# Performance work log

Hardware: AMD Instinct MI355X
Metric: run time of the kernel (lower is better)

Reference implementation:

```python
import jax, jax.numpy as jnp
import numpy as np

N = 200000       # nodes
E = 6400000      # edges
F_IN, H1, H2, C = 7, 32, 16, 2


def gcn_conv(x, W, b, src, dst, n):
    """PyG GCNConv: add self-loops, symmetric normalization, linear, scatter-add."""
    loop = jnp.arange(n, dtype=src.dtype)
    s = jnp.concatenate([src, loop])
    d = jnp.concatenate([dst, loop])
    # degree of target nodes (with self-loops)
    deg = jax.ops.segment_sum(jnp.ones_like(d, dtype=x.dtype), d, num_segments=n)
    dinv = jnp.where(deg > 0, jax.lax.rsqrt(deg), 0.0)
    h = x @ W                                  # [n, out]
    norm = dinv[s] * dinv[d]                   # [e+n]
    msg = h[s] * norm[:, None]                 # gather + normalize
    out = jax.ops.segment_sum(msg, d, num_segments=n)  # scatter-add aggregation
    return out + b


def setup_inputs() -> dict:
    key = jax.random.key(0)
    ks = jax.random.split(key, 8)
    x = jax.random.normal(ks[0], (N, F_IN), dtype=jnp.float32)
    edge_index = jax.random.randint(ks[1], (2, E), 0, N, dtype=jnp.int64)
    def glorot(k, fan_in, fan_out):
        lim = np.sqrt(6.0 / (fan_in + fan_out)).astype(np.float32)
        return jax.random.uniform(k, (fan_in, fan_out), jnp.float32, -lim, lim)
    return {
        "x": x,
        "edge_index": edge_index,
        "W1": glorot(ks[2], F_IN, H1), "b1": jnp.zeros((H1,), jnp.float32),
        "W2": glorot(ks[3], H1, H2), "b2": jnp.zeros((H2,), jnp.float32),
        "Wfc": glorot(ks[4], H2, C), "bfc": jnp.zeros((C,), jnp.float32),
    }


def reference(x, edge_index, W1, b1, W2, b2, Wfc, bfc):
    src, dst = edge_index[0], edge_index[1]
    h = jax.nn.relu(gcn_conv(x, W1, b1, src, dst, N))
    h = jax.nn.relu(gcn_conv(h, W2, b2, src, dst, N))
    return h @ Wfc + bfc
```

## Files before the change

### kernel.cpp

```cpp
#include <hip/hip_runtime.h>

#define NNODES 200000
#define NEDGES 6400000
#define FIN 7
#define FH1 32
#define FH2 16
#define NC 2

#define WB 128
#define WB_SHIFT 7
#define NBUCK ((NNODES + WB - 1) / WB)
#define NBLK 512
#define CHUNK ((NEDGES + NBLK - 1) / NBLK)
#define PSHIFT 18
#define SRCMASK ((1u << PSHIFT) - 1)

#define SCAP 5120

#define SCAN_N (NBUCK * NBLK)
#define SCAN_ITEMS 16
#define SCAN_TILE (256 * SCAN_ITEMS)
#define SCAN_NT ((SCAN_N + SCAN_TILE - 1) / SCAN_TILE)


__global__ __launch_bounds__(256) void p1_count(const int* __restrict__ ei,
                                                int* __restrict__ counts) {
    __shared__ int h[NBUCK];
    for (int i = threadIdx.x; i < NBUCK; i += 256) h[i] = 0;
    __syncthreads();
    int base = blockIdx.x * CHUNK;
    int end = base + CHUNK;
    if (end > NEDGES) end = NEDGES;
    for (int e = base + threadIdx.x; e < end; e += 256) {
        int d = ei[NEDGES + e];
        atomicAdd(&h[d >> WB_SHIFT], 1);
    }
    __syncthreads();
    for (int i = threadIdx.x; i < NBUCK; i += 256)
        counts[i * NBLK + blockIdx.x] = h[i];
}


__global__ __launch_bounds__(256) void scan_sums(const int* __restrict__ in,
                                                 int* __restrict__ part) {
    int base = blockIdx.x * SCAN_TILE + threadIdx.x * SCAN_ITEMS;
    int s = 0;
#pragma unroll
    for (int k = 0; k < SCAN_ITEMS; ++k) {
        int idx = base + k;
        if (idx < SCAN_N) s += in[idx];
    }
    __shared__ int sm[256];
    sm[threadIdx.x] = s;
    __syncthreads();
    for (int off = 128; off > 0; off >>= 1) {
        if (threadIdx.x < off) sm[threadIdx.x] += sm[threadIdx.x + off];
        __syncthreads();
    }
    if (threadIdx.x == 0) part[blockIdx.x] = sm[0];
}

__global__ void scan_top_g(int* __restrict__ part) {
    if (threadIdx.x == 0 && blockIdx.x == 0) {
        int acc = 0;
        for (int i = 0; i < SCAN_NT; ++i) {
            int v = part[i];
            part[i] = acc;
            acc += v;
        }
    }
}

__global__ __launch_bounds__(256) void scan_write_g(const int* __restrict__ in,
                                                    const int* __restrict__ part,
                                                    int* __restrict__ out) {
    int t = threadIdx.x;
    int base = blockIdx.x * SCAN_TILE + t * SCAN_ITEMS;
    int local[SCAN_ITEMS];
    int s = 0;
#pragma unroll
    for (int k = 0; k < SCAN_ITEMS; ++k) {
        int idx = base + k;
        int v = (idx < SCAN_N) ? in[idx] : 0;
        local[k] = v;
        s += v;
    }
    __shared__ int sm[256];
    sm[t] = s;
    __syncthreads();
    for (int off = 1; off < 256; off <<= 1) {
        int v = (t >= off) ? sm[t - off] : 0;
        __syncthreads();
        sm[t] += v;
        __syncthreads();
    }
    int prefix = part[blockIdx.x] + sm[t] - s;
#pragma unroll
    for (int k = 0; k < SCAN_ITEMS; ++k) {
        int idx = base + k;
        if (idx < SCAN_N) {
            out[idx] = prefix;
            prefix += local[k];
        }
    }
}


__global__ __launch_bounds__(256) void p2_scatter(const int* __restrict__ ei,
                                                  const int* __restrict__ offs,
                                                  unsigned int* __restrict__ recs) {
    __shared__ int sorted[CHUNK];
    __shared__ int lcur[NBUCK];
    __shared__ int gbase[NBUCK];
    __shared__ int sm[256];
    int t = threadIdx.x;
    int blk = blockIdx.x;

    for (int b = t; b < NBUCK; b += 256) {
        int g = offs[b * NBLK + blk];
        gbase[b] = g;
        int nxt;
        if (blk + 1 < NBLK) nxt = offs[b * NBLK + blk + 1];
        else nxt = (b + 1 < NBUCK) ? offs[(b + 1) * NBLK] : NEDGES;
        lcur[b] = nxt - g;
    }
    __syncthreads();

    int base7 = t * 7;
    int loc[7];
    int s = 0;
#pragma unroll
    for (int k = 0; k < 7; ++k) {
        int idx = base7 + k;
        int v = (idx < NBUCK) ? lcur[idx] : 0;
        loc[k] = v;
        s += v;
    }
    sm[t] = s;
    __syncthreads();
    for (int off = 1; off < 256; off <<= 1) {
        int v = (t >= off) ? sm[t - off] : 0;
        __syncthreads();
        sm[t] += v;
        __syncthreads();
    }
    int run = sm[t] - s;
#pragma unroll
    for (int k = 0; k < 7; ++k) {
        int idx = base7 + k;
        if (idx < NBUCK) { lcur[idx] = run; run += loc[k]; }
    }
    __syncthreads();

    int ebase = blk * CHUNK;
    for (int e = ebase + t; e < ebase + CHUNK; e += 256) {
        int src = ei[e];
        int d = ei[NEDGES + e];
        int b = d >> WB_SHIFT;
        int slot = atomicAdd(&lcur[b], 1);
        sorted[slot] = (int)((unsigned)src | ((unsigned)(d & (WB - 1)) << PSHIFT));
    }
    __syncthreads();

    for (int i = t; i < CHUNK; i += 256) {
        int lo = 0, hi = NBUCK - 1;
        while (lo < hi) {
            int mid = (lo + hi) >> 1;
            if (lcur[mid] > i) hi = mid; else lo = mid + 1;
        }
        int b = lo;
        int start = (b > 0) ? lcur[b - 1] : 0;
        recs[gbase[b] + (i - start)] = (unsigned)sorted[i];
    }
}


__global__ __launch_bounds__(256) void p3_dinv(const unsigned int* __restrict__ recs,
                                               const int* __restrict__ offs,
                                               float* __restrict__ dinv) {
    __shared__ int h[WB];
    int b = blockIdx.x;
    if (threadIdx.x < WB) h[threadIdx.x] = 0;
    __syncthreads();
    int beg = offs[b * NBLK];
    int end = (b + 1 < NBUCK) ? offs[(b + 1) * NBLK] : NEDGES;
    for (int e = beg + threadIdx.x; e < end; e += 256)
        atomicAdd(&h[recs[e] >> PSHIFT], 1);
    __syncthreads();
    int node = b * WB + threadIdx.x;
    if (threadIdx.x < WB && node < NNODES)
        dinv[node] = rsqrtf((float)(1 + h[threadIdx.x]));
}


__global__ __launch_bounds__(256) void gx_kernel(const float* __restrict__ x,
                                                 const float* __restrict__ dinv,
                                                 float4* __restrict__ gx) {
    int i = blockIdx.x * blockDim.x + threadIdx.x;
    if (i >= NNODES) return;
    float di = dinv[i];
    const float* xr = x + (size_t)i * FIN;
    float4 v0, v1;
    v0.x = xr[0] * di; v0.y = xr[1] * di; v0.z = xr[2] * di; v0.w = xr[3] * di;
    v1.x = xr[4] * di; v1.y = xr[5] * di; v1.z = xr[6] * di; v1.w = 0.0f;
    gx[(size_t)i * 2 + 0] = v0;
    gx[(size_t)i * 2 + 1] = v1;
}


__global__ __launch_bounds__(256) void l1_sorted(const unsigned int* __restrict__ recs,
                                                 const int* __restrict__ offs,
                                                 const float4* __restrict__ gx,
                                                 const float* __restrict__ dinv,
                                                 const float* __restrict__ W1,
                                                 const float* __restrict__ b1,
                                                 const float* __restrict__ W2,
                                                 float4* __restrict__ y) {
    __shared__ int sl_src[SCAP];
    __shared__ int hist[WB], st[WB], cur[WB];
    __shared__ float acc[WB][9];
    __shared__ float sW1[FIN * FH1];
    __shared__ float sb1[FH1];
    __shared__ float sW2[FH1 * FH2];
    int t = threadIdx.x;
    for (int i = t; i < FIN * FH1; i += 256) sW1[i] = W1[i];
    if (t < FH1) sb1[t] = b1[t];
    for (int i = t; i < FH1 * FH2; i += 256) sW2[i] = W2[i];
    if (t < WB) hist[t] = 0;
    __syncthreads();

    int b = blockIdx.x;
    int beg = offs[b * NBLK];
    int end = (b + 1 < NBUCK) ? offs[(b + 1) * NBLK] : NEDGES;

    for (int e = beg + t; e < end; e += 256)
        atomicAdd(&hist[recs[e] >> PSHIFT], 1);
    __syncthreads();

    if (t < WB) cur[t] = hist[t];
    __syncthreads();
    for (int off = 1; off < WB; off <<= 1) {
        int v = 0;
        if (t < WB && t >= off) v = cur[t - off];
        __syncthreads();
        if (t < WB) cur[t] += v;
        __syncthreads();
    }
    if (t < WB) {
        st[t] = cur[t] - hist[t];
        cur[t] = cur[t] - hist[t];
    }
    __syncthreads();

    for (int e = beg + t; e < end; e += 256) {
        unsigned r = recs[e];
        int slot = atomicAdd(&cur[r >> PSHIFT], 1);
        sl_src[slot] = (int)(r & SRCMASK);
    }
    __syncthreads();

    int n = t >> 1;
    int hq = t & 1;
    int cnt = hist[n];
    int base = st[n];
    float ax = 0.0f, ay = 0.0f, az = 0.0f, aw = 0.0f;
    int k = 0;
    for (; k + 3 < cnt; k += 4) {
        int s0 = sl_src[base + k];
        int s1 = sl_src[base + k + 1];
        int s2 = sl_src[base + k + 2];
        int s3 = sl_src[base + k + 3];
        float4 v0 = gx[(size_t)s0 * 2 + hq];
        float4 v1 = gx[(size_t)s1 * 2 + hq];
        float4 v2 = gx[(size_t)s2 * 2 + hq];
        float4 v3 = gx[(size_t)s3 * 2 + hq];
        ax += v0.x + v1.x; ay += v0.y + v1.y;
        az += v0.z + v1.z; aw += v0.w + v1.w;
        ax += v2.x + v3.x; ay += v2.y + v3.y;
        az += v2.z + v3.z; aw += v2.w + v3.w;
    }
    for (; k < cnt; ++k) {
        int s0 = sl_src[base + k];
        float4 v0 = gx[(size_t)s0 * 2 + hq];
        ax += v0.x; ay += v0.y; az += v0.z; aw += v0.w;
    }
    int kb = hq * 4;
    acc[n][kb + 0] = ax; acc[n][kb + 1] = ay;
    acc[n][kb + 2] = az; acc[n][kb + 3] = aw;
    __syncthreads();

    int node = b * WB + t;
    if (t >= WB || node >= NNODES) return;

    float di = dinv[node];
    float4 g0 = gx[(size_t)node * 2], g1 = gx[(size_t)node * 2 + 1];
    float xa[FIN];
    xa[0] = (acc[t][0] + g0.x) * di;
    xa[1] = (acc[t][1] + g0.y) * di;
    xa[2] = (acc[t][2] + g0.z) * di;
    xa[3] = (acc[t][3] + g0.w) * di;
    xa[4] = (acc[t][4] + g1.x) * di;
    xa[5] = (acc[t][5] + g1.y) * di;
    xa[6] = (acc[t][6] + g1.z) * di;

    float h1[FH1];
#pragma unroll
    for (int j = 0; j < FH1; ++j) h1[j] = sb1[j];
#pragma unroll
    for (int f = 0; f < FIN; ++f) {
        float xv = xa[f];
#pragma unroll
        for (int j = 0; j < FH1; ++j) h1[j] = fmaf(xv, sW1[f * FH1 + j], h1[j]);
    }
#pragma unroll
    for (int j = 0; j < FH1; ++j) h1[j] = fmaxf(h1[j], 0.0f);

    float yv[FH2];
#pragma unroll
    for (int j = 0; j < FH2; ++j) yv[j] = 0.0f;
#pragma unroll
    for (int k2 = 0; k2 < FH1; ++k2) {
        float hv = h1[k2];
#pragma unroll
        for (int j = 0; j < FH2; ++j) yv[j] = fmaf(hv, sW2[k2 * FH2 + j], yv[j]);
    }

    size_t yb = (size_t)node * 4;
    float4 o;
    o.x = yv[0] * di; o.y = yv[1] * di; o.z = yv[2] * di; o.w = yv[3] * di;
    y[yb + 0] = o;
    o.x = yv[4] * di; o.y = yv[5] * di; o.z = yv[6] * di; o.w = yv[7] * di;
    y[yb + 1] = o;
    o.x = yv[8] * di; o.y = yv[9] * di; o.z = yv[10] * di; o.w = yv[11] * di;
    y[yb + 2] = o;
    o.x = yv[12] * di; o.y = yv[13] * di; o.z = yv[14] * di; o.w = yv[15] * di;
    y[yb + 3] = o;
}


__global__ __launch_bounds__(256) void l2_sorted(const unsigned int* __restrict__ recs,
                                                 const int* __restrict__ offs,
                                                 const float4* __restrict__ y,
                                                 const float* __restrict__ dinv,
                                                 const float* __restrict__ b2,
                                                 const float* __restrict__ Wfc,
                                                 const float* __restrict__ bfc,
                                                 float2* __restrict__ out) {
    __shared__ int sl_src[SCAP];
    __shared__ int hist[WB], st[WB], cur[WB];
    __shared__ float acc[WB][17];
    __shared__ float sb2[FH2];
    __shared__ float sWfc[FH2 * NC];
    __shared__ float sbfc[NC];
    int t = threadIdx.x;
    if (t < FH2) sb2[t] = b2[t];
    if (t < FH2 * NC) sWfc[t] = Wfc[t];
    if (t < NC) sbfc[t] = bfc[t];
    if (t < WB) hist[t] = 0;
    __syncthreads();

    int b = blockIdx.x;
    int beg = offs[b * NBLK];
    int end = (b + 1 < NBUCK) ? offs[(b + 1) * NBLK] : NEDGES;

    for (int e = beg + t; e < end; e += 256)
        atomicAdd(&hist[recs[e] >> PSHIFT], 1);
    __syncthreads();

    if (t < WB) cur[t] = hist[t];
    __syncthreads();
    for (int off = 1; off < WB; off <<= 1) {
        int v = 0;
        if (t < WB && t >= off) v = cur[t - off];
        __syncthreads();
        if (t < WB) cur[t] += v;
        __syncthreads();
    }
    if (t < WB) {
        st[t] = cur[t] - hist[t];
        cur[t] = cur[t] - hist[t];
    }
    __syncthreads();

    for (int e = beg + t; e < end; e += 256) {
        unsigned r = recs[e];
        int slot = atomicAdd(&cur[r >> PSHIFT], 1);
        sl_src[slot] = (int)(r & SRCMASK);
    }
    __syncthreads();

    int q = t & 3;
#pragma unroll
    for (int r = 0; r < 2; ++r) {
        int n = (t >> 2) + 64 * r;
        int cnt = hist[n];
        int base = st[n];
        float ax = 0.0f, ay = 0.0f, az = 0.0f, aw = 0.0f;
        int k = 0;
        for (; k + 3 < cnt; k += 4) {
            int s0 = sl_src[base + k];
            int s1 = sl_src[base + k + 1];
            int s2 = sl_src[base + k + 2];
            int s3 = sl_src[base + k + 3];
            float4 v0 = y[(size_t)s0 * 4 + q];
            float4 v1 = y[(size_t)s1 * 4 + q];
            float4 v2 = y[(size_t)s2 * 4 + q];
            float4 v3 = y[(size_t)s3 * 4 + q];
            ax += v0.x + v1.x; ay += v0.y + v1.y;
            az += v0.z + v1.z; aw += v0.w + v1.w;
            ax += v2.x + v3.x; ay += v2.y + v3.y;
            az += v2.z + v3.z; aw += v2.w + v3.w;
        }
        for (; k < cnt; ++k) {
            int s0 = sl_src[base + k];
            float4 v0 = y[(size_t)s0 * 4 + q];
            ax += v0.x; ay += v0.y; az += v0.z; aw += v0.w;
        }
        int kb = q * 4;
        acc[n][kb + 0] = ax; acc[n][kb + 1] = ay;
        acc[n][kb + 2] = az; acc[n][kb + 3] = aw;
    }
    __syncthreads();

    int node = b * WB + t;
    if (t >= WB || node >= NNODES) return;

    float di = dinv[node];
    size_t yb = (size_t)node * 4;
    float4 s0 = y[yb + 0], s1 = y[yb + 1], s2 = y[yb + 2], s3 = y[yb + 3];
    float self[FH2] = {s0.x, s0.y, s0.z, s0.w, s1.x, s1.y, s1.z, s1.w,
                       s2.x, s2.y, s2.z, s2.w, s3.x, s3.y, s3.z, s3.w};

    float o0 = sbfc[0], o1 = sbfc[1];
#pragma unroll
    for (int k = 0; k < FH2; ++k) {
        float h = fmaxf(fmaf(di, acc[t][k] + self[k], sb2[k]), 0.0f);
        o0 = fmaf(h, sWfc[k * NC + 0], o0);
        o1 = fmaf(h, sWfc[k * NC + 1], o1);
    }
    float2 ov; ov.x = o0; ov.y = o1;
    out[node] = ov;
}


extern "C" void kernel_launch(void* const* d_in, const int* in_sizes, int n_in,
                              void* d_out, int out_size, void* d_ws, size_t ws_size,
                              hipStream_t stream) {
    const float* x   = (const float*)d_in[0];
    const int*   ei  = (const int*)d_in[1];
    const float* W1  = (const float*)d_in[2];
    const float* b1  = (const float*)d_in[3];
    const float* W2  = (const float*)d_in[4];
    const float* b2  = (const float*)d_in[5];
    const float* Wfc = (const float*)d_in[6];
    const float* bfc = (const float*)d_in[7];
    float* out = (float*)d_out;

    char* p = (char*)d_ws;
    auto carve = [&](size_t bytes) -> char* {
        char* r = p;
        p += (bytes + 255) & ~(size_t)255;
        return r;
    };
    int*      counts = (int*)carve((size_t)SCAN_N * 4);
    int*      part   = (int*)carve(256 * 4);
    float*    dinv   = (float*)carve((size_t)NNODES * 4);
    float*    gx     = (float*)carve((size_t)NNODES * 8 * 4);
    float*    y      = (float*)carve((size_t)NNODES * 16 * 4);
    unsigned* recs   = (unsigned*)carve((size_t)NEDGES * 4);
    int* offs = counts;

    int nblocks = (NNODES + 255) / 256;

    p1_count<<<NBLK, 256, 0, stream>>>(ei, counts);
    scan_sums<<<SCAN_NT, 256, 0, stream>>>(counts, part);
    scan_top_g<<<1, 64, 0, stream>>>(part);
    scan_write_g<<<SCAN_NT, 256, 0, stream>>>(counts, part, offs);
    p2_scatter<<<NBLK, 256, 0, stream>>>(ei, offs, recs);
    p3_dinv<<<NBUCK, 256, 0, stream>>>(recs, offs, dinv);
    gx_kernel<<<nblocks, 256, 0, stream>>>(x, dinv, (float4*)gx);
    l1_sorted<<<NBUCK, 256, 0, stream>>>(recs, offs, (const float4*)gx, dinv,
                                         W1, b1, W2, (float4*)y);
    l2_sorted<<<NBUCK, 256, 0, stream>>>(recs, offs, (const float4*)y, dinv,
                                         b2, Wfc, bfc, (float2*)out);
}
```

Baseline: 382.1 us.

## Sort edges per node once in a fused pass and reuse CSR offsets in both layers

A new pass, p2b_sort, does the within-bucket counting sort once. It writes the fully node-sorted source indices back into recs, builds a per-node CSR offset array, and computes the dinv-scaled input features, replacing the separate dinv and gx kernels. The two layer kernels then skip their own histogram, scan and shared-memory scatter. They just copy the contiguous slice into shared memory and recompute dinv from the offsets. This removes duplicated edge passes and shared atomics in l1 and l2, at the cost of one extra write of recs.

```diff
diff --git a/kernel.cpp b/kernel.cpp
--- a/kernel.cpp
+++ b/kernel.cpp
@@ -175,49 +175,75 @@
 }
 
 
-__global__ __launch_bounds__(256) void p3_dinv(const unsigned int* __restrict__ recs,
-                                               const int* __restrict__ offs,
-                                               float* __restrict__ dinv) {
-    __shared__ int h[WB];
+__global__ __launch_bounds__(256) void p2b_sort(unsigned int* __restrict__ recs,
+                                                const int* __restrict__ offs,
+                                                const float* __restrict__ x,
+                                                int* __restrict__ node_off,
+                                                float4* __restrict__ gx) {
+    __shared__ int sorted[SCAP];
+    __shared__ int hist[WB], st[WB], cur[WB];
+    int t = threadIdx.x;
     int b = blockIdx.x;
-    if (threadIdx.x < WB) h[threadIdx.x] = 0;
-    __syncthreads();
+    if (t < WB) hist[t] = 0;
+    __syncthreads();
+
     int beg = offs[b * NBLK];
     int end = (b + 1 < NBUCK) ? offs[(b + 1) * NBLK] : NEDGES;
-    for (int e = beg + threadIdx.x; e < end; e += 256)
-        atomicAdd(&h[recs[e] >> PSHIFT], 1);
-    __syncthreads();
-    int node = b * WB + threadIdx.x;
-    if (threadIdx.x < WB && node < NNODES)
-        dinv[node] = rsqrtf((float)(1 + h[threadIdx.x]));
-}
-
-
-__global__ __launch_bounds__(256) void gx_kernel(const float* __restrict__ x,
-                                                 const float* __restrict__ dinv,
-                                                 float4* __restrict__ gx) {
-    int i = blockIdx.x * blockDim.x + threadIdx.x;
-    if (i >= NNODES) return;
-    float di = dinv[i];
-    const float* xr = x + (size_t)i * FIN;
-    float4 v0, v1;
-    v0.x = xr[0] * di; v0.y = xr[1] * di; v0.z = xr[2] * di; v0.w = xr[3] * di;
-    v1.x = xr[4] * di; v1.y = xr[5] * di; v1.z = xr[6] * di; v1.w = 0.0f;
-    gx[(size_t)i * 2 + 0] = v0;
-    gx[(size_t)i * 2 + 1] = v1;
-}
-
-
-__global__ __launch_bounds__(256) void l1_sorted(const unsigned int* __restrict__ recs,
-                                                 const int* __restrict__ offs,
-                                                 const float4* __restrict__ gx,
-                                                 const float* __restrict__ dinv,
-                                                 const float* __restrict__ W1,
-                                                 const float* __restrict__ b1,
-                                                 const float* __restrict__ W2,
-                                                 float4* __restrict__ y) {
+
+    for (int e = beg + t; e < end; e += 256)
+        atomicAdd(&hist[recs[e] >> PSHIFT], 1);
+    __syncthreads();
+
+    if (t < WB) cur[t] = hist[t];
+    __syncthreads();
+    for (int off = 1; off < WB; off <<= 1) {
+        int v = 0;
+        if (t < WB && t >= off) v = cur[t - off];
+        __syncthreads();
+        if (t < WB) cur[t] += v;
+        __syncthreads();
+    }
+    if (t < WB) {
+        st[t] = cur[t] - hist[t];
+        cur[t] = st[t];
+    }
+    __syncthreads();
+
+    for (int e = beg + t; e < end; e += 256) {
+        unsigned r = recs[e];
+        int slot = atomicAdd(&cur[r >> PSHIFT], 1);
+        sorted[slot] = (int)(r & SRCMASK);
+    }
+    __syncthreads();
+
+    int cnt = end - beg;
+    for (int i = t; i < cnt; i += 256)
+        recs[beg + i] = (unsigned)sorted[i];
+
+    int node = b * WB + t;
+    if (t < WB && node < NNODES) {
+        node_off[node] = beg + st[t];
+        float di = rsqrtf((float)(1 + hist[t]));
+        const float* xr = x + (size_t)node * FIN;
+        float4 v0, v1;
+        v0.x = xr[0] * di; v0.y = xr[1] * di; v0.z = xr[2] * di; v0.w = xr[3] * di;
+        v1.x = xr[4] * di; v1.y = xr[5] * di; v1.z = xr[6] * di; v1.w = 0.0f;
+        gx[(size_t)node * 2 + 0] = v0;
+        gx[(size_t)node * 2 + 1] = v1;
+    }
+    if (b == 0 && t == 0) node_off[NNODES] = NEDGES;
+}
+
+
+__global__ __launch_bounds__(256) void l1_fast(const unsigned int* __restrict__ recs,
+                                               const int* __restrict__ node_off,
+                                               const float4* __restrict__ gx,
+                                               const float* __restrict__ W1,
+                                               const float* __restrict__ b1,
+                                               const float* __restrict__ W2,
+                                               float4* __restrict__ y) {
     __shared__ int sl_src[SCAP];
-    __shared__ int hist[WB], st[WB], cur[WB];
+    __shared__ int noffs[WB + 1];
     __shared__ float acc[WB][9];
     __shared__ float sW1[FIN * FH1];
     __shared__ float sb1[FH1];
@@ -226,43 +252,23 @@
     for (int i = t; i < FIN * FH1; i += 256) sW1[i] = W1[i];
     if (t < FH1) sb1[t] = b1[t];
     for (int i = t; i < FH1 * FH2; i += 256) sW2[i] = W2[i];
-    if (t < WB) hist[t] = 0;
-    __syncthreads();
 
     int b = blockIdx.x;
-    int beg = offs[b * NBLK];
-    int end = (b + 1 < NBUCK) ? offs[(b + 1) * NBLK] : NEDGES;
-
-    for (int e = beg + t; e < end; e += 256)
-        atomicAdd(&hist[recs[e] >> PSHIFT], 1);
-    __syncthreads();
-
-    if (t < WB) cur[t] = hist[t];
-    __syncthreads();
-    for (int off = 1; off < WB; off <<= 1) {
-        int v = 0;
-        if (t < WB && t >= off) v = cur[t - off];
-        __syncthreads();
-        if (t < WB) cur[t] += v;
-        __syncthreads();
-    }
-    if (t < WB) {
-        st[t] = cur[t] - hist[t];
-        cur[t] = cur[t] - hist[t];
-    }
-    __syncthreads();
-
-    for (int e = beg + t; e < end; e += 256) {
-        unsigned r = recs[e];
-        int slot = atomicAdd(&cur[r >> PSHIFT], 1);
-        sl_src[slot] = (int)(r & SRCMASK);
-    }
+    for (int i = t; i <= WB; i += 256) {
+        int idx = b * WB + i;
+        noffs[i] = (idx >= NNODES) ? NEDGES : node_off[idx];
+    }
+    __syncthreads();
+
+    int beg = noffs[0];
+    int cnt_all = noffs[WB] - beg;
+    for (int i = t; i < cnt_all; i += 256) sl_src[i] = (int)recs[beg + i];
     __syncthreads();
 
     int n = t >> 1;
     int hq = t & 1;
-    int cnt = hist[n];
-    int base = st[n];
+    int base = noffs[n] - beg;
+    int cnt = noffs[n + 1] - noffs[n];
     float ax = 0.0f, ay = 0.0f, az = 0.0f, aw = 0.0f;
     int k = 0;
     for (; k + 3 < cnt; k += 4) {
@@ -292,7 +298,7 @@
     int node = b * WB + t;
     if (t >= WB || node >= NNODES) return;
 
-    float di = dinv[node];
+    float di = rsqrtf((float)(1 + (noffs[t + 1] - noffs[t])));
     float4 g0 = gx[(size_t)node * 2], g1 = gx[(size_t)node * 2 + 1];
     float xa[FIN];
     xa[0] = (acc[t][0] + g0.x) * di;
@@ -338,16 +344,15 @@
 }
 
 
-__global__ __launch_bounds__(256) void l2_sorted(const unsigned int* __restrict__ recs,
-                                                 const int* __restrict__ offs,
-                                                 const float4* __restrict__ y,
-                                                 const float* __restrict__ dinv,
-                                                 const float* __restrict__ b2,
-                                                 const float* __restrict__ Wfc,
-                                                 const float* __restrict__ bfc,
-                                                 float2* __restrict__ out) {
+__global__ __launch_bounds__(256) void l2_fast(const unsigned int* __restrict__ recs,
+                                               const int* __restrict__ node_off,
+                                               const float4* __restrict__ y,
+                                               const float* __restrict__ b2,
+                                               const float* __restrict__ Wfc,
+                                               const float* __restrict__ bfc,
+                                               float2* __restrict__ out) {
     __shared__ int sl_src[SCAP];
-    __shared__ int hist[WB], st[WB], cur[WB];
+    __shared__ int noffs[WB + 1];
     __shared__ float acc[WB][17];
     __shared__ float sb2[FH2];
     __shared__ float sWfc[FH2 * NC];
@@ -356,45 +361,25 @@
     if (t < FH2) sb2[t] = b2[t];
     if (t < FH2 * NC) sWfc[t] = Wfc[t];
     if (t < NC) sbfc[t] = bfc[t];
-    if (t < WB) hist[t] = 0;
-    __syncthreads();
 
     int b = blockIdx.x;
-    int beg = offs[b * NBLK];
-    int end = (b + 1 < NBUCK) ? offs[(b + 1) * NBLK] : NEDGES;
-
-    for (int e = beg + t; e < end; e += 256)
-        atomicAdd(&hist[recs[e] >> PSHIFT], 1);
-    __syncthreads();
-
-    if (t < WB) cur[t] = hist[t];
-    __syncthreads();
-    for (int off = 1; off < WB; off <<= 1) {
-        int v = 0;
-        if (t < WB && t >= off) v = cur[t - off];
-        __syncthreads();
-        if (t < WB) cur[t] += v;
-        __syncthreads();
-    }
-    if (t < WB) {
-        st[t] = cur[t] - hist[t];
-        cur[t] = cur[t] - hist[t];
-    }
-    __syncthreads();
-
-    for (int e = beg + t; e < end; e += 256) {
-        unsigned r = recs[e];
-        int slot = atomicAdd(&cur[r >> PSHIFT], 1);
-        sl_src[slot] = (int)(r & SRCMASK);
-    }
+    for (int i = t; i <= WB; i += 256) {
+        int idx = b * WB + i;
+        noffs[i] = (idx >= NNODES) ? NEDGES : node_off[idx];
+    }
+    __syncthreads();
+
+    int beg = noffs[0];
+    int cnt_all = noffs[WB] - beg;
+    for (int i = t; i < cnt_all; i += 256) sl_src[i] = (int)recs[beg + i];
     __syncthreads();
 
     int q = t & 3;
 #pragma unroll
     for (int r = 0; r < 2; ++r) {
         int n = (t >> 2) + 64 * r;
-        int cnt = hist[n];
-        int base = st[n];
+        int base = noffs[n] - beg;
+        int cnt = noffs[n + 1] - noffs[n];
         float ax = 0.0f, ay = 0.0f, az = 0.0f, aw = 0.0f;
         int k = 0;
         for (; k + 3 < cnt; k += 4) {
@@ -425,7 +410,7 @@
     int node = b * WB + t;
     if (t >= WB || node >= NNODES) return;
 
-    float di = dinv[node];
+    float di = rsqrtf((float)(1 + (noffs[t + 1] - noffs[t])));
     size_t yb = (size_t)node * 4;
     float4 s0 = y[yb + 0], s1 = y[yb + 1], s2 = y[yb + 2], s3 = y[yb + 3];
     float self[FH2] = {s0.x, s0.y, s0.z, s0.w, s1.x, s1.y, s1.z, s1.w,
@@ -462,25 +447,22 @@
         p += (bytes + 255) & ~(size_t)255;
         return r;
     };
-    int*      counts = (int*)carve((size_t)SCAN_N * 4);
-    int*      part   = (int*)carve(256 * 4);
-    float*    dinv   = (float*)carve((size_t)NNODES * 4);
-    float*    gx     = (float*)carve((size_t)NNODES * 8 * 4);
-    float*    y      = (float*)carve((size_t)NNODES * 16 * 4);
-    unsigned* recs   = (unsigned*)carve((size_t)NEDGES * 4);
+    int*      counts   = (int*)carve((size_t)SCAN_N * 4);
+    int*      part     = (int*)carve(256 * 4);
+    int*      node_off = (int*)carve((size_t)(NNODES + 1) * 4);
+    float*    gx       = (float*)carve((size_t)NNODES * 8 * 4);
+    float*    y        = (float*)carve((size_t)NNODES * 16 * 4);
+    unsigned* recs     = (unsigned*)carve((size_t)NEDGES * 4);
     int* offs = counts;
-
-    int nblocks = (NNODES + 255) / 256;
 
     p1_count<<<NBLK, 256, 0, stream>>>(ei, counts);
     scan_sums<<<SCAN_NT, 256, 0, stream>>>(counts, part);
     scan_top_g<<<1, 64, 0, stream>>>(part);
     scan_write_g<<<SCAN_NT, 256, 0, stream>>>(counts, part, offs);
     p2_scatter<<<NBLK, 256, 0, stream>>>(ei, offs, recs);
-    p3_dinv<<<NBUCK, 256, 0, stream>>>(recs, offs, dinv);
-    gx_kernel<<<nblocks, 256, 0, stream>>>(x, dinv, (float4*)gx);
-    l1_sorted<<<NBUCK, 256, 0, stream>>>(recs, offs, (const float4*)gx, dinv,
-                                         W1, b1, W2, (float4*)y);
-    l2_sorted<<<NBUCK, 256, 0, stream>>>(recs, offs, (const float4*)y, dinv,
-                                         b2, Wfc, bfc, (float2*)out);
-}
+    p2b_sort<<<NBUCK, 256, 0, stream>>>(recs, offs, x, node_off, (float4*)gx);
+    l1_fast<<<NBUCK, 256, 0, stream>>>(recs, node_off, (const float4*)gx,
+                                       W1, b1, W2, (float4*)y);
+    l2_fast<<<NBUCK, 256, 0, stream>>>(recs, node_off, (const float4*)y,
+                                       b2, Wfc, bfc, (float2*)out);
+}
```

Result: no change. 375.4 us (-1.8%).
